# Optimization experiments

Hardware: AMD Instinct MI355X
Metric: run time of the kernel (lower is better)

Reference implementation:

```python
import jax, jax.numpy as jnp
import numpy as np


def setup_inputs() -> dict:
    key = jax.random.key(0)
    kq, kk, kv, km = jax.random.split(key, 4)
    B, H, S, D = 4, 16, 2048, 64
    query = jax.random.normal(kq, (B, H, S, D), dtype=jnp.float32)
    k = jax.random.normal(kk, (B, H, S, D), dtype=jnp.float32)
    value = jax.random.normal(kv, (B, H, S, D), dtype=jnp.float32)
    mask = jax.random.randint(km, (B, S, S), 0, 2, dtype=jnp.int32)
    return {"query": query, "key": k, "value": value, "mask": mask}


def reference(query, key, value, mask):
    # query/key/value: [B, H, S, D]; mask: [B, S, S] (0 = masked out)
    d = query.shape[-1]
    scale = 1.0 / jnp.sqrt(jnp.asarray(d, dtype=query.dtype))
    scores = jnp.einsum('bhqd,bhkd->bhqk', query, key) * scale
    m = (mask[:, None, :, :] == 0)  # broadcast over heads, matches mask.unsqueeze(1).eq(0)
    min_value = jnp.finfo(scores.dtype).min
    scores = jnp.where(m, min_value, scores)
    attn = jax.nn.softmax(scores, axis=-1)
    attn = jnp.where(m, jnp.asarray(0.0, attn.dtype), attn)
    out = jnp.einsum('bhqk,bhkd->bhqd', attn, value)
    return (out, attn)
```

## Files before the change

### kernel.cpp

```cpp
#include <hip/hip_runtime.h>


typedef __attribute__((ext_vector_type(8))) short bf16x8;
typedef __attribute__((ext_vector_type(4))) float f32x4;
typedef __attribute__((ext_vector_type(4))) int i32x4;
typedef __attribute__((ext_vector_type(2))) unsigned int u32x2;

#define MFMA16(A, B, C) __builtin_amdgcn_mfma_f32_16x16x32_bf16((A), (B), (C), 0, 0, 0)

constexpr int Bsz = 4, Hsz = 16, Ssz = 2048, Dsz = 64;
constexpr int QBLK = 64;
constexpr int KBLK = 64;
constexpr int NTHR = 512;
constexpr int NT   = Ssz / KBLK;
constexpr float SCALE = 0.125f;

static __device__ __forceinline__ short f2bf(float f) {
  unsigned u = __float_as_uint(f);
  u = (u + 0x7fffu + ((u >> 16) & 1u)) >> 16;
  return (short)u;
}

static __device__ __forceinline__ void wg_barrier() {
  __builtin_amdgcn_sched_barrier(0);
  asm volatile("s_waitcnt lgkmcnt(0)" ::: "memory");
  __builtin_amdgcn_sched_barrier(0);
  __builtin_amdgcn_s_barrier();
  __builtin_amdgcn_sched_barrier(0);
}

__global__ __launch_bounds__(NTHR, 4)
void attn_fused(const float* __restrict__ Qg, const float* __restrict__ Kg,
                const float* __restrict__ Vg, const int* __restrict__ Mg,
                float* __restrict__ Og, float* __restrict__ Ag)
{
  __shared__ __align__(16) char smem[5 * 64 * 72 * 2];
  auto sK  = (short(*)[KBLK][72])(smem);
  auto sVt = (short(*)[Dsz][72])(smem + 2 * 9216);
  auto sP  = (short(*)[72])(smem + 4 * 9216);
  auto sO  = (float(*)[68])(smem);
  __shared__ float sL[2][QBLK];

  const int qt   = blockIdx.x;
  const int bh   = blockIdx.y;
  const int q0   = qt * QBLK;
  const int tid  = threadIdx.x;
  const int lane = tid & 63;
  const int wid  = tid >> 6;
  const int wq   = wid >> 1;
  const int wk   = wid & 1;
  const int lr   = lane & 15;
  const int lg   = lane >> 4;

  const size_t bhSD = (size_t)bh * (Ssz * Dsz);
  const float* Qb = Qg + bhSD;
  const float* Kb = Kg + bhSD;
  const float* Vb = Vg + bhSD;
  const int*   Mb = Mg + (size_t)(bh >> 4) * ((size_t)Ssz * Ssz);
  float*       Ob = Og + bhSD;
  float*       Ab = Ag + (size_t)bh * ((size_t)Ssz * Ssz);

  const int qrow = q0 + wq * 16 + lr;
  const int* Mrow = Mb + (size_t)qrow * Ssz;
  float*     Arow = Ab + (size_t)qrow * Ssz;

  bf16x8 qf[2];
  {
    const float* qp = Qb + (size_t)qrow * Dsz + lg * 8;
#pragma unroll
    for (int h = 0; h < 2; ++h) {
      f32x4 a = *(const f32x4*)(qp + h * 32);
      f32x4 b = *(const f32x4*)(qp + h * 32 + 4);
      bf16x8 t;
#pragma unroll
      for (int j = 0; j < 4; ++j) { t[j] = f2bf(a[j] * SCALE); t[4 + j] = f2bf(b[j] * SCALE); }
      qf[h] = t;
    }
  }

  const int krow = tid >> 3;
  const int kd0  = (tid & 7) * 8;
  const int vkv  = tid & 63;
  const int vd0  = (tid >> 6) * 8;
  const int kb0  = wk * 32 + lg * 4;

  {
    const float* kp = Kb + (size_t)krow * Dsz + kd0;
    f32x4 a = *(const f32x4*)kp;
    f32x4 b = *(const f32x4*)(kp + 4);
    bf16x8 t;
#pragma unroll
    for (int j = 0; j < 4; ++j) { t[j] = f2bf(a[j]); t[4 + j] = f2bf(b[j]); }
    *(bf16x8*)(&sK[0][krow][kd0]) = t;
  }
  i32x4 m0n = *(const i32x4*)(Mrow + kb0);
  i32x4 m1n = *(const i32x4*)(Mrow + kb0 + 16);
  wg_barrier();

  float lacc = 0.f;
  for (int t = 0; t < NT; ++t) {
    const int cur = t & 1;
    const i32x4 m0 = m0n, m1 = m1n;
    f32x4 ka = {0.f, 0.f, 0.f, 0.f}, kb2 = {0.f, 0.f, 0.f, 0.f};
    if (t + 1 < NT) {
      const float* kp = Kb + (size_t)((t + 1) * KBLK + krow) * Dsz + kd0;
      ka  = *(const f32x4*)kp;
      kb2 = *(const f32x4*)(kp + 4);
      m0n = *(const i32x4*)(Mrow + (t + 1) * KBLK + kb0);
      m1n = *(const i32x4*)(Mrow + (t + 1) * KBLK + kb0 + 16);
    }
#pragma unroll
    for (int cb = 0; cb < 2; ++cb) {
      const short* kr = &sK[cur][wk * 32 + cb * 16 + lr][0];
      bf16x8 a0 = *(const bf16x8*)(kr + lg * 8);
      bf16x8 a1 = *(const bf16x8*)(kr + 32 + lg * 8);
      f32x4 c = {0.f, 0.f, 0.f, 0.f};
      c = MFMA16(a0, qf[0], c);
      c = MFMA16(a1, qf[1], c);
      i32x4 mv = cb ? m1 : m0;
#pragma unroll
      for (int r = 0; r < 4; ++r) lacc += mv[r] ? __expf(c[r]) : 0.f;
    }
    if (t + 1 < NT) {
      bf16x8 tt;
#pragma unroll
      for (int j = 0; j < 4; ++j) { tt[j] = f2bf(ka[j]); tt[4 + j] = f2bf(kb2[j]); }
      *(bf16x8*)(&sK[cur ^ 1][krow][kd0]) = tt;
    }
    wg_barrier();
  }

  lacc += __shfl_xor(lacc, 16, 64);
  lacc += __shfl_xor(lacc, 32, 64);
  if (lane < 16) sL[wk][wq * 16 + lane] = lacc;
  wg_barrier();
  const float lsum = sL[0][wq * 16 + lr] + sL[1][wq * 16 + lr];
  const float invl = (lsum > 0.f) ? 1.f / lsum : 0.f;

  f32x4 oacc[4] = {{0,0,0,0},{0,0,0,0},{0,0,0,0},{0,0,0,0}};

  {
    const float* kp = Kb + (size_t)krow * Dsz + kd0;
    f32x4 a = *(const f32x4*)kp;
    f32x4 b = *(const f32x4*)(kp + 4);
    bf16x8 t;
#pragma unroll
    for (int j = 0; j < 4; ++j) { t[j] = f2bf(a[j]); t[4 + j] = f2bf(b[j]); }
    *(bf16x8*)(&sK[0][krow][kd0]) = t;

    const float* vp = Vb + (size_t)vkv * Dsz + vd0;
    f32x4 va = *(const f32x4*)vp;
    f32x4 vb = *(const f32x4*)(vp + 4);
#pragma unroll
    for (int j = 0; j < 4; ++j) {
      sVt[0][vd0 + j][vkv]     = f2bf(va[j]);
      sVt[0][vd0 + 4 + j][vkv] = f2bf(vb[j]);
    }
  }
  m0n = *(const i32x4*)(Mrow + kb0);
  m1n = *(const i32x4*)(Mrow + kb0 + 16);
  wg_barrier();

  for (int t = 0; t < NT; ++t) {
    const int cur = t & 1;
    const i32x4 m0 = m0n, m1 = m1n;
    f32x4 ka = {0.f,0.f,0.f,0.f}, kb2 = {0.f,0.f,0.f,0.f};
    f32x4 va = {0.f,0.f,0.f,0.f}, vb2 = {0.f,0.f,0.f,0.f};
    if (t + 1 < NT) {
      const float* kp = Kb + (size_t)((t + 1) * KBLK + krow) * Dsz + kd0;
      ka  = *(const f32x4*)kp;
      kb2 = *(const f32x4*)(kp + 4);
      const float* vp = Vb + (size_t)((t + 1) * KBLK + vkv) * Dsz + vd0;
      va  = *(const f32x4*)vp;
      vb2 = *(const f32x4*)(vp + 4);
      m0n = *(const i32x4*)(Mrow + (t + 1) * KBLK + kb0);
      m1n = *(const i32x4*)(Mrow + (t + 1) * KBLK + kb0 + 16);
    }
#pragma unroll
    for (int cb = 0; cb < 2; ++cb) {
      const short* kr = &sK[cur][wk * 32 + cb * 16 + lr][0];
      bf16x8 a0 = *(const bf16x8*)(kr + lg * 8);
      bf16x8 a1 = *(const bf16x8*)(kr + 32 + lg * 8);
      f32x4 c = {0.f, 0.f, 0.f, 0.f};
      c = MFMA16(a0, qf[0], c);
      c = MFMA16(a1, qf[1], c);
      i32x4 mv = cb ? m1 : m0;
      f32x4 p;
#pragma unroll
      for (int r = 0; r < 4; ++r) p[r] = mv[r] ? __expf(c[r]) * invl : 0.f;
      __builtin_nontemporal_store(p, (f32x4*)(Arow + t * KBLK + kb0 + cb * 16));
      unsigned plo = (unsigned short)f2bf(p[0]) | ((unsigned)(unsigned short)f2bf(p[1]) << 16);
      unsigned phi = (unsigned short)f2bf(p[2]) | ((unsigned)(unsigned short)f2bf(p[3]) << 16);
      u32x2 w = {plo, phi};
      *(u32x2*)(&sP[wq * 16 + lr][wk * 32 + cb * 16 + lg * 4]) = w;
    }
    bf16x8 pa = *(const bf16x8*)(&sP[wq * 16 + lr][wk * 32 + lg * 8]);
#pragma unroll
    for (int nb = 0; nb < 4; ++nb) {
      bf16x8 vb = *(const bf16x8*)(&sVt[cur][nb * 16 + lr][wk * 32 + lg * 8]);
      oacc[nb] = MFMA16(pa, vb, oacc[nb]);
    }
    if (t + 1 < NT) {
      bf16x8 tt;
#pragma unroll
      for (int j = 0; j < 4; ++j) { tt[j] = f2bf(ka[j]); tt[4 + j] = f2bf(kb2[j]); }
      *(bf16x8*)(&sK[cur ^ 1][krow][kd0]) = tt;
#pragma unroll
      for (int j = 0; j < 4; ++j) {
        sVt[cur ^ 1][vd0 + j][vkv]     = f2bf(va[j]);
        sVt[cur ^ 1][vd0 + 4 + j][vkv] = f2bf(vb2[j]);
      }
    }
    wg_barrier();
  }

  if (wk == 0) {
#pragma unroll
    for (int nb = 0; nb < 4; ++nb)
#pragma unroll
      for (int r = 0; r < 4; ++r)
        sO[wq * 16 + lg * 4 + r][nb * 16 + lr] = oacc[nb][r];
  }
  wg_barrier();
  if (wk == 1) {
#pragma unroll
    for (int nb = 0; nb < 4; ++nb)
#pragma unroll
      for (int r = 0; r < 4; ++r) {
        float v = sO[wq * 16 + lg * 4 + r][nb * 16 + lr] + oacc[nb][r];
        __builtin_nontemporal_store(v, Ob + (size_t)(q0 + wq * 16 + lg * 4 + r) * Dsz + nb * 16 + lr);
      }
  }
}

extern "C" void kernel_launch(void* const* d_in, const int* in_sizes, int n_in,
                              void* d_out, int out_size, void* d_ws, size_t ws_size,
                              hipStream_t stream) {
  const float* Q = (const float*)d_in[0];
  const float* K = (const float*)d_in[1];
  const float* V = (const float*)d_in[2];
  const int*   M = (const int*)d_in[3];
  float* Out  = (float*)d_out;
  float* Attn = Out + (size_t)Bsz * Hsz * Ssz * Dsz;
  dim3 grid(Ssz / QBLK, Bsz * Hsz);
  attn_fused<<<grid, NTHR, 0, stream>>>(Q, K, V, M, Out, Attn);
}
```

Measured before the change: 503.0 us.

## Load K fragments directly from global in softmax-denominator pass, drop LDS staging and barriers

The first pass, which accumulates the softmax denominator, now has each lane load its K fragment straight from global memory into registers and convert it to bf16, with software prefetch of the next 16-row chunk. This removes the LDS staging writes and the per-tile workgroup barriers from that pass. Each K element is now loaded redundantly by several waves, which relies on cache hits and raises global/L2 traffic. The f2bf helper is also switched to the HIP library conversion.

```diff
diff --git a/kernel.cpp b/kernel.cpp
--- a/kernel.cpp
+++ b/kernel.cpp
@@ -1,4 +1,5 @@
 #include <hip/hip_runtime.h>
+#include <hip/hip_bf16.h>
 
 
 typedef __attribute__((ext_vector_type(8))) short bf16x8;
@@ -13,12 +14,12 @@
 constexpr int KBLK = 64;
 constexpr int NTHR = 512;
 constexpr int NT   = Ssz / KBLK;
+constexpr int NH   = 64;
 constexpr float SCALE = 0.125f;
 
 static __device__ __forceinline__ short f2bf(float f) {
-  unsigned u = __float_as_uint(f);
-  u = (u + 0x7fffu + ((u >> 16) & 1u)) >> 16;
-  return (short)u;
+  __hip_bfloat16 h = __float2bfloat16(f);
+  return __builtin_bit_cast(short, h);
 }
 
 static __device__ __forceinline__ void wg_barrier() {
@@ -78,56 +79,53 @@
     }
   }
 
-  const int krow = tid >> 3;
-  const int kd0  = (tid & 7) * 8;
-  const int vkv  = tid & 63;
-  const int vd0  = (tid >> 6) * 8;
-  const int kb0  = wk * 32 + lg * 4;
-
+  float lacc = 0.f;
   {
-    const float* kp = Kb + (size_t)krow * Dsz + kd0;
-    f32x4 a = *(const f32x4*)kp;
-    f32x4 b = *(const f32x4*)(kp + 4);
-    bf16x8 t;
-#pragma unroll
-    for (int j = 0; j < 4; ++j) { t[j] = f2bf(a[j]); t[4 + j] = f2bf(b[j]); }
-    *(bf16x8*)(&sK[0][krow][kd0]) = t;
-  }
-  i32x4 m0n = *(const i32x4*)(Mrow + kb0);
-  i32x4 m1n = *(const i32x4*)(Mrow + kb0 + 16);
-  wg_barrier();
-
-  float lacc = 0.f;
-  for (int t = 0; t < NT; ++t) {
-    const int cur = t & 1;
-    const i32x4 m0 = m0n, m1 = m1n;
-    f32x4 ka = {0.f, 0.f, 0.f, 0.f}, kb2 = {0.f, 0.f, 0.f, 0.f};
-    if (t + 1 < NT) {
-      const float* kp = Kb + (size_t)((t + 1) * KBLK + krow) * Dsz + kd0;
-      ka  = *(const f32x4*)kp;
-      kb2 = *(const f32x4*)(kp + 4);
-      m0n = *(const i32x4*)(Mrow + (t + 1) * KBLK + kb0);
-      m1n = *(const i32x4*)(Mrow + (t + 1) * KBLK + kb0 + 16);
-    }
-#pragma unroll
-    for (int cb = 0; cb < 2; ++cb) {
-      const short* kr = &sK[cur][wk * 32 + cb * 16 + lr][0];
-      bf16x8 a0 = *(const bf16x8*)(kr + lg * 8);
-      bf16x8 a1 = *(const bf16x8*)(kr + 32 + lg * 8);
+    const float* Klane = Kb + (size_t)lr * Dsz + lg * 8;
+    const int*   Mlane = Mrow + lg * 4;
+
+    f32x4 L[4]; i32x4 mc;
+    {
+      const int koff = wk * 32;
+      const float* kp = Klane + (size_t)koff * Dsz;
+      L[0] = *(const f32x4*)(kp);
+      L[1] = *(const f32x4*)(kp + 4);
+      L[2] = *(const f32x4*)(kp + 32);
+      L[3] = *(const f32x4*)(kp + 36);
+      mc = *(const i32x4*)(Mlane + koff);
+    }
+    bf16x8 F0, F1;
+#pragma unroll
+    for (int j = 0; j < 4; ++j) {
+      F0[j] = f2bf(L[0][j]); F0[4 + j] = f2bf(L[1][j]);
+      F1[j] = f2bf(L[2][j]); F1[4 + j] = f2bf(L[3][j]);
+    }
+
+    for (int h = 0; h < NH; ++h) {
+      f32x4 Ln[4]; i32x4 mn;
+      if (h + 1 < NH) {
+        const int koff = ((h + 1) >> 1) * 64 + wk * 32 + ((h + 1) & 1) * 16;
+        const float* kp = Klane + (size_t)koff * Dsz;
+        Ln[0] = *(const f32x4*)(kp);
+        Ln[1] = *(const f32x4*)(kp + 4);
+        Ln[2] = *(const f32x4*)(kp + 32);
+        Ln[3] = *(const f32x4*)(kp + 36);
+        mn = *(const i32x4*)(Mlane + koff);
+      }
       f32x4 c = {0.f, 0.f, 0.f, 0.f};
-      c = MFMA16(a0, qf[0], c);
-      c = MFMA16(a1, qf[1], c);
-      i32x4 mv = cb ? m1 : m0;
-#pragma unroll
-      for (int r = 0; r < 4; ++r) lacc += mv[r] ? __expf(c[r]) : 0.f;
-    }
-    if (t + 1 < NT) {
-      bf16x8 tt;
-#pragma unroll
-      for (int j = 0; j < 4; ++j) { tt[j] = f2bf(ka[j]); tt[4 + j] = f2bf(kb2[j]); }
-      *(bf16x8*)(&sK[cur ^ 1][krow][kd0]) = tt;
-    }
-    wg_barrier();
+      c = MFMA16(F0, qf[0], c);
+      c = MFMA16(F1, qf[1], c);
+#pragma unroll
+      for (int r = 0; r < 4; ++r) lacc += mc[r] ? __expf(c[r]) : 0.f;
+      if (h + 1 < NH) {
+#pragma unroll
+        for (int j = 0; j < 4; ++j) {
+          F0[j] = f2bf(Ln[0][j]); F0[4 + j] = f2bf(Ln[1][j]);
+          F1[j] = f2bf(Ln[2][j]); F1[4 + j] = f2bf(Ln[3][j]);
+        }
+        mc = mn;
+      }
+    }
   }
 
   lacc += __shfl_xor(lacc, 16, 64);
@@ -137,6 +135,12 @@
   const float lsum = sL[0][wq * 16 + lr] + sL[1][wq * 16 + lr];
   const float invl = (lsum > 0.f) ? 1.f / lsum : 0.f;
 
+  const int krow = tid >> 3;
+  const int kd0  = (tid & 7) * 8;
+  const int vkv  = tid & 63;
+  const int vd0  = (tid >> 6) * 8;
+  const int kb0  = wk * 32 + lg * 4;
+
   f32x4 oacc[4] = {{0,0,0,0},{0,0,0,0},{0,0,0,0},{0,0,0,0}};
 
   {
@@ -157,8 +161,8 @@
       sVt[0][vd0 + 4 + j][vkv] = f2bf(vb[j]);
     }
   }
-  m0n = *(const i32x4*)(Mrow + kb0);
-  m1n = *(const i32x4*)(Mrow + kb0 + 16);
+  i32x4 m0n = *(const i32x4*)(Mrow + kb0);
+  i32x4 m1n = *(const i32x4*)(Mrow + kb0 + 16);
   wg_barrier();
 
   for (int t = 0; t < NT; ++t) {
```

Result: slower. 915.7 us (+82.1%).

## Split attention into denominator and emit kernels with bit-packed mask workspace

Applied to the files above, without the earlier changes.

Splits the fused two-pass kernel into a denominator kernel that computes inverse softmax sums and packs the int32 mask into bits in workspace, and an emit kernel that reads those bits instead of the full int32 mask. This removes the second full mask read per head, cutting global traffic in the output pass. It also raises occupancy hints, switches to the library bf16 conversion, and adds s_setprio around the MFMA section. Every head redundantly writes identical mask bits, and an extra launch plus workspace round trip is added.

```diff
diff --git a/kernel.cpp b/kernel.cpp
--- a/kernel.cpp
+++ b/kernel.cpp
@@ -1,4 +1,5 @@
 #include <hip/hip_runtime.h>
+#include <hip/hip_bf16.h>
 
 
 typedef __attribute__((ext_vector_type(8))) short bf16x8;
@@ -9,16 +10,13 @@
 #define MFMA16(A, B, C) __builtin_amdgcn_mfma_f32_16x16x32_bf16((A), (B), (C), 0, 0, 0)
 
 constexpr int Bsz = 4, Hsz = 16, Ssz = 2048, Dsz = 64;
-constexpr int QBLK = 64;
 constexpr int KBLK = 64;
-constexpr int NTHR = 512;
 constexpr int NT   = Ssz / KBLK;
 constexpr float SCALE = 0.125f;
 
 static __device__ __forceinline__ short f2bf(float f) {
-  unsigned u = __float_as_uint(f);
-  u = (u + 0x7fffu + ((u >> 16) & 1u)) >> 16;
-  return (short)u;
+  __hip_bfloat16 h = __float2bfloat16(f);
+  return __builtin_bit_cast(short, h);
 }
 
 static __device__ __forceinline__ void wg_barrier() {
@@ -29,40 +27,123 @@
   __builtin_amdgcn_sched_barrier(0);
 }
 
-__global__ __launch_bounds__(NTHR, 4)
-void attn_fused(const float* __restrict__ Qg, const float* __restrict__ Kg,
-                const float* __restrict__ Vg, const int* __restrict__ Mg,
-                float* __restrict__ Og, float* __restrict__ Ag)
+__global__ __launch_bounds__(512, 8)
+void attn_denom(const float* __restrict__ Qg, const float* __restrict__ Kg,
+                const int* __restrict__ Mg, float* __restrict__ wsL,
+                unsigned short* __restrict__ wsM)
+{
+  __shared__ short sK[2][KBLK][72];
+
+  const int qt = blockIdx.x, bh = blockIdx.y;
+  const int q0 = qt * 128;
+  const int tid = threadIdx.x, lane = tid & 63, w = tid >> 6;
+  const int lr = lane & 15, lg = lane >> 4;
+
+  const size_t bhSD = (size_t)bh * (Ssz * Dsz);
+  const float* Qb = Qg + bhSD;
+  const float* Kb = Kg + bhSD;
+  const int b = bh >> 4;
+  const int qrow = q0 + w * 16 + lr;
+  const int* Mrow = Mg + ((size_t)b * Ssz + qrow) * Ssz;
+  unsigned short* wsMq = wsM + (size_t)(b * Ssz + qrow) * (NT * 4) + lg;
+
+  bf16x8 qf[2];
+  {
+    const float* qp = Qb + (size_t)qrow * Dsz + lg * 8;
+#pragma unroll
+    for (int h = 0; h < 2; ++h) {
+      f32x4 a = *(const f32x4*)(qp + h * 32);
+      f32x4 c2 = *(const f32x4*)(qp + h * 32 + 4);
+      bf16x8 t;
+#pragma unroll
+      for (int j = 0; j < 4; ++j) { t[j] = f2bf(a[j] * SCALE); t[4 + j] = f2bf(c2[j] * SCALE); }
+      qf[h] = t;
+    }
+  }
+
+  const int krow = tid >> 3, kd0 = (tid & 7) * 8;
+  {
+    const float* kp = Kb + (size_t)krow * Dsz + kd0;
+    f32x4 a = *(const f32x4*)kp, c2 = *(const f32x4*)(kp + 4);
+    bf16x8 t;
+#pragma unroll
+    for (int j = 0; j < 4; ++j) { t[j] = f2bf(a[j]); t[4 + j] = f2bf(c2[j]); }
+    *(bf16x8*)(&sK[0][krow][kd0]) = t;
+  }
+  wg_barrier();
+
+  float lacc = 0.f;
+  for (int t = 0; t < NT; ++t) {
+    const int cur = t & 1;
+    f32x4 ka = {0.f,0.f,0.f,0.f}, kb2 = {0.f,0.f,0.f,0.f};
+    if (t + 1 < NT) {
+      const float* kp = Kb + (size_t)((t + 1) * KBLK + krow) * Dsz + kd0;
+      ka  = *(const f32x4*)kp;
+      kb2 = *(const f32x4*)(kp + 4);
+    }
+    unsigned bits = 0;
+#pragma unroll
+    for (int cb = 0; cb < 4; ++cb) {
+      const short* kr = &sK[cur][cb * 16 + lr][0];
+      bf16x8 a0 = *(const bf16x8*)(kr + lg * 8);
+      bf16x8 a1 = *(const bf16x8*)(kr + 32 + lg * 8);
+      f32x4 c = {0.f, 0.f, 0.f, 0.f};
+      c = MFMA16(a0, qf[0], c);
+      c = MFMA16(a1, qf[1], c);
+      i32x4 mv = *(const i32x4*)(Mrow + t * KBLK + cb * 16 + lg * 4);
+#pragma unroll
+      for (int r = 0; r < 4; ++r) {
+        lacc += mv[r] ? __expf(c[r]) : 0.f;
+        bits |= (mv[r] ? 1u : 0u) << (cb * 4 + r);
+      }
+    }
+    wsMq[t * 4] = (unsigned short)bits;
+    if (t + 1 < NT) {
+      bf16x8 t2;
+#pragma unroll
+      for (int j = 0; j < 4; ++j) { t2[j] = f2bf(ka[j]); t2[4 + j] = f2bf(kb2[j]); }
+      *(bf16x8*)(&sK[cur ^ 1][krow][kd0]) = t2;
+    }
+    wg_barrier();
+  }
+
+  lacc += __shfl_xor(lacc, 16, 64);
+  lacc += __shfl_xor(lacc, 32, 64);
+  if (lane < 16)
+    wsL[(size_t)bh * Ssz + qrow] = (lacc > 0.f) ? 1.f / lacc : 0.f;
+}
+
+__global__ __launch_bounds__(512, 6)
+void attn_emit(const float* __restrict__ Qg, const float* __restrict__ Kg,
+               const float* __restrict__ Vg, const float* __restrict__ wsL,
+               const unsigned short* __restrict__ wsM,
+               float* __restrict__ Og, float* __restrict__ Ag)
 {
   __shared__ __align__(16) char smem[5 * 64 * 72 * 2];
   auto sK  = (short(*)[KBLK][72])(smem);
   auto sVt = (short(*)[Dsz][72])(smem + 2 * 9216);
   auto sP  = (short(*)[72])(smem + 4 * 9216);
   auto sO  = (float(*)[68])(smem);
-  __shared__ float sL[2][QBLK];
-
-  const int qt   = blockIdx.x;
-  const int bh   = blockIdx.y;
-  const int q0   = qt * QBLK;
-  const int tid  = threadIdx.x;
-  const int lane = tid & 63;
-  const int wid  = tid >> 6;
-  const int wq   = wid >> 1;
-  const int wk   = wid & 1;
-  const int lr   = lane & 15;
-  const int lg   = lane >> 4;
+
+  const int qt = blockIdx.x, bh = blockIdx.y;
+  const int q0 = qt * 64;
+  const int tid = threadIdx.x, lane = tid & 63, wid = tid >> 6;
+  const int wq = wid >> 1, wk = wid & 1;
+  const int lr = lane & 15, lg = lane >> 4;
 
   const size_t bhSD = (size_t)bh * (Ssz * Dsz);
   const float* Qb = Qg + bhSD;
   const float* Kb = Kg + bhSD;
   const float* Vb = Vg + bhSD;
-  const int*   Mb = Mg + (size_t)(bh >> 4) * ((size_t)Ssz * Ssz);
-  float*       Ob = Og + bhSD;
-  float*       Ab = Ag + (size_t)bh * ((size_t)Ssz * Ssz);
+  const int b = bh >> 4;
+  float* Ob = Og + bhSD;
+  float* Ab = Ag + (size_t)bh * ((size_t)Ssz * Ssz);
 
   const int qrow = q0 + wq * 16 + lr;
-  const int* Mrow = Mb + (size_t)qrow * Ssz;
-  float*     Arow = Ab + (size_t)qrow * Ssz;
+  float* Arow = Ab + (size_t)qrow * Ssz;
+  const float invl = wsL[(size_t)bh * Ssz + qrow];
+  const unsigned short* wsMq = wsM + (size_t)(b * Ssz + qrow) * (NT * 4) + lg;
+  const int mshift = wk * 8;
 
   bf16x8 qf[2];
   {
@@ -70,10 +151,10 @@
 #pragma unroll
     for (int h = 0; h < 2; ++h) {
       f32x4 a = *(const f32x4*)(qp + h * 32);
-      f32x4 b = *(const f32x4*)(qp + h * 32 + 4);
+      f32x4 c2 = *(const f32x4*)(qp + h * 32 + 4);
       bf16x8 t;
 #pragma unroll
-      for (int j = 0; j < 4; ++j) { t[j] = f2bf(a[j] * SCALE); t[4 + j] = f2bf(b[j] * SCALE); }
+      for (int j = 0; j < 4; ++j) { t[j] = f2bf(a[j] * SCALE); t[4 + j] = f2bf(c2[j] * SCALE); }
       qf[h] = t;
     }
   }
@@ -84,31 +165,42 @@
   const int vd0  = (tid >> 6) * 8;
   const int kb0  = wk * 32 + lg * 4;
 
+  f32x4 oacc[4] = {{0,0,0,0},{0,0,0,0},{0,0,0,0},{0,0,0,0}};
+
   {
     const float* kp = Kb + (size_t)krow * Dsz + kd0;
-    f32x4 a = *(const f32x4*)kp;
-    f32x4 b = *(const f32x4*)(kp + 4);
+    f32x4 a = *(const f32x4*)kp, c2 = *(const f32x4*)(kp + 4);
     bf16x8 t;
 #pragma unroll
-    for (int j = 0; j < 4; ++j) { t[j] = f2bf(a[j]); t[4 + j] = f2bf(b[j]); }
+    for (int j = 0; j < 4; ++j) { t[j] = f2bf(a[j]); t[4 + j] = f2bf(c2[j]); }
     *(bf16x8*)(&sK[0][krow][kd0]) = t;
-  }
-  i32x4 m0n = *(const i32x4*)(Mrow + kb0);
-  i32x4 m1n = *(const i32x4*)(Mrow + kb0 + 16);
+
+    const float* vp = Vb + (size_t)vkv * Dsz + vd0;
+    f32x4 va = *(const f32x4*)vp, vb = *(const f32x4*)(vp + 4);
+#pragma unroll
+    for (int j = 0; j < 4; ++j) {
+      sVt[0][vd0 + j][vkv]     = f2bf(va[j]);
+      sVt[0][vd0 + 4 + j][vkv] = f2bf(vb[j]);
+    }
+  }
+  unsigned mbn = wsMq[0];
   wg_barrier();
 
-  float lacc = 0.f;
   for (int t = 0; t < NT; ++t) {
     const int cur = t & 1;
-    const i32x4 m0 = m0n, m1 = m1n;
-    f32x4 ka = {0.f, 0.f, 0.f, 0.f}, kb2 = {0.f, 0.f, 0.f, 0.f};
+    const unsigned mb = mbn;
+    f32x4 ka = {0.f,0.f,0.f,0.f}, kb2 = {0.f,0.f,0.f,0.f};
+    f32x4 va = {0.f,0.f,0.f,0.f}, vb2 = {0.f,0.f,0.f,0.f};
     if (t + 1 < NT) {
       const float* kp = Kb + (size_t)((t + 1) * KBLK + krow) * Dsz + kd0;
       ka  = *(const f32x4*)kp;
       kb2 = *(const f32x4*)(kp + 4);
-      m0n = *(const i32x4*)(Mrow + (t + 1) * KBLK + kb0);
-      m1n = *(const i32x4*)(Mrow + (t + 1) * KBLK + kb0 + 16);
-    }
+      const float* vp = Vb + (size_t)((t + 1) * KBLK + vkv) * Dsz + vd0;
+      va  = *(const f32x4*)vp;
+      vb2 = *(const f32x4*)(vp + 4);
+      mbn = wsMq[(t + 1) * 4];
+    }
+    __builtin_amdgcn_s_setprio(1);
 #pragma unroll
     for (int cb = 0; cb < 2; ++cb) {
       const short* kr = &sK[cur][wk * 32 + cb * 16 + lr][0];
@@ -117,82 +209,15 @@
       f32x4 c = {0.f, 0.f, 0.f, 0.f};
       c = MFMA16(a0, qf[0], c);
       c = MFMA16(a1, qf[1], c);
-      i32x4 mv = cb ? m1 : m0;
-#pragma unroll
-      for (int r = 0; r < 4; ++r) lacc += mv[r] ? __expf(c[r]) : 0.f;
-    }
-    if (t + 1 < NT) {
-      bf16x8 tt;
-#pragma unroll
-      for (int j = 0; j < 4; ++j) { tt[j] = f2bf(ka[j]); tt[4 + j] = f2bf(kb2[j]); }
-      *(bf16x8*)(&sK[cur ^ 1][krow][kd0]) = tt;
-    }
-    wg_barrier();
-  }
-
-  lacc += __shfl_xor(lacc, 16, 64);
-  lacc += __shfl_xor(lacc, 32, 64);
-  if (lane < 16) sL[wk][wq * 16 + lane] = lacc;
-  wg_barrier();
-  const float lsum = sL[0][wq * 16 + lr] + sL[1][wq * 16 + lr];
-  const float invl = (lsum > 0.f) ? 1.f / lsum : 0.f;
-
-  f32x4 oacc[4] = {{0,0,0,0},{0,0,0,0},{0,0,0,0},{0,0,0,0}};
-
-  {
-    const float* kp = Kb + (size_t)krow * Dsz + kd0;
-    f32x4 a = *(const f32x4*)kp;
-    f32x4 b = *(const f32x4*)(kp + 4);
-    bf16x8 t;
-#pragma unroll
-    for (int j = 0; j < 4; ++j) { t[j] = f2bf(a[j]); t[4 + j] = f2bf(b[j]); }
-    *(bf16x8*)(&sK[0][krow][kd0]) = t;
-
-    const float* vp = Vb + (size_t)vkv * Dsz + vd0;
-    f32x4 va = *(const f32x4*)vp;
-    f32x4 vb = *(const f32x4*)(vp + 4);
-#pragma unroll
-    for (int j = 0; j < 4; ++j) {
-      sVt[0][vd0 + j][vkv]     = f2bf(va[j]);
-      sVt[0][vd0 + 4 + j][vkv] = f2bf(vb[j]);
-    }
-  }
-  m0n = *(const i32x4*)(Mrow + kb0);
-  m1n = *(const i32x4*)(Mrow + kb0 + 16);
-  wg_barrier();
-
-  for (int t = 0; t < NT; ++t) {
-    const int cur = t & 1;
-    const i32x4 m0 = m0n, m1 = m1n;
-    f32x4 ka = {0.f,0.f,0.f,0.f}, kb2 = {0.f,0.f,0.f,0.f};
-    f32x4 va = {0.f,0.f,0.f,0.f}, vb2 = {0.f,0.f,0.f,0.f};
-    if (t + 1 < NT) {
-      const float* kp = Kb + (size_t)((t + 1) * KBLK + krow) * Dsz + kd0;
-      ka  = *(const f32x4*)kp;
-      kb2 = *(const f32x4*)(kp + 4);
-      const float* vp = Vb + (size_t)((t + 1) * KBLK + vkv) * Dsz + vd0;
-      va  = *(const f32x4*)vp;
-      vb2 = *(const f32x4*)(vp + 4);
-      m0n = *(const i32x4*)(Mrow + (t + 1) * KBLK + kb0);
-      m1n = *(const i32x4*)(Mrow + (t + 1) * KBLK + kb0 + 16);
-    }
-#pragma unroll
-    for (int cb = 0; cb < 2; ++cb) {
-      const short* kr = &sK[cur][wk * 32 + cb * 16 + lr][0];
-      bf16x8 a0 = *(const bf16x8*)(kr + lg * 8);
-      bf16x8 a1 = *(const bf16x8*)(kr + 32 + lg * 8);
-      f32x4 c = {0.f, 0.f, 0.f, 0.f};
-      c = MFMA16(a0, qf[0], c);
-      c = MFMA16(a1, qf[1], c);
-      i32x4 mv = cb ? m1 : m0;
       f32x4 p;
 #pragma unroll
-      for (int r = 0; r < 4; ++r) p[r] = mv[r] ? __expf(c[r]) * invl : 0.f;
+      for (int r = 0; r < 4; ++r)
+        p[r] = ((mb >> (mshift + cb * 4 + r)) & 1u) ? __expf(c[r]) * invl : 0.f;
       __builtin_nontemporal_store(p, (f32x4*)(Arow + t * KBLK + kb0 + cb * 16));
       unsigned plo = (unsigned short)f2bf(p[0]) | ((unsigned)(unsigned short)f2bf(p[1]) << 16);
       unsigned phi = (unsigned short)f2bf(p[2]) | ((unsigned)(unsigned short)f2bf(p[3]) << 16);
-      u32x2 w = {plo, phi};
-      *(u32x2*)(&sP[wq * 16 + lr][wk * 32 + cb * 16 + lg * 4]) = w;
+      u32x2 wv = {plo, phi};
+      *(u32x2*)(&sP[wq * 16 + lr][wk * 32 + cb * 16 + lg * 4]) = wv;
     }
     bf16x8 pa = *(const bf16x8*)(&sP[wq * 16 + lr][wk * 32 + lg * 8]);
 #pragma unroll
@@ -200,11 +225,12 @@
       bf16x8 vb = *(const bf16x8*)(&sVt[cur][nb * 16 + lr][wk * 32 + lg * 8]);
       oacc[nb] = MFMA16(pa, vb, oacc[nb]);
     }
-    if (t + 1 < NT) {
-      bf16x8 tt;
-#pragma unroll
-      for (int j = 0; j < 4; ++j) { tt[j] = f2bf(ka[j]); tt[4 + j] = f2bf(kb2[j]); }
-      *(bf16x8*)(&sK[cur ^ 1][krow][kd0]) = tt;
+    __builtin_amdgcn_s_setprio(0);
+    if (t + 1 < NT) {
+      bf16x8 t2;
+#pragma unroll
+      for (int j = 0; j < 4; ++j) { t2[j] = f2bf(ka[j]); t2[4 + j] = f2bf(kb2[j]); }
+      *(bf16x8*)(&sK[cur ^ 1][krow][kd0]) = t2;
 #pragma unroll
       for (int j = 0; j < 4; ++j) {
         sVt[cur ^ 1][vd0 + j][vkv]     = f2bf(va[j]);
@@ -242,6 +268,8 @@
   const int*   M = (const int*)d_in[3];
   float* Out  = (float*)d_out;
   float* Attn = Out + (size_t)Bsz * Hsz * Ssz * Dsz;
-  dim3 grid(Ssz / QBLK, Bsz * Hsz);
-  attn_fused<<<grid, NTHR, 0, stream>>>(Q, K, V, M, Out, Attn);
-}
+  float* wsL = (float*)d_ws;
+  unsigned short* wsM = (unsigned short*)((char*)d_ws + (size_t)Bsz * Hsz * Ssz * sizeof(float));
+  attn_denom<<<dim3(Ssz / 128, Bsz * Hsz), 512, 0, stream>>>(Q, K, M, wsL, wsM);
+  attn_emit <<<dim3(Ssz / 64,  Bsz * Hsz), 512, 0, stream>>>(Q, K, V, wsL, wsM, Out, Attn);
+}
```

Result: no change. 504.8 us (+0.4%).
